# Performance work log

Hardware: AMD Instinct MI355X
Metric: run time of the kernel (lower is better)

The kernel has to match this reference:

```python
import jax, jax.numpy as jnp
import numpy as np

EPS = 0.2          # noise scale (init eps)
N_LAYERS = 3
LAYER_CL = 1
USER_NUM = 100000
ITEM_NUM = 50000
NNZ = 1200000
EMB = 64


def setup_inputs() -> dict:
    key = jax.random.key(0)
    k1, k2, k3, k4, k5, k6 = jax.random.split(key, 6)
    N = USER_NUM + ITEM_NUM
    user_emb = jax.random.normal(k1, (USER_NUM, EMB), dtype=jnp.float32)
    item_emb = jax.random.normal(k2, (ITEM_NUM, EMB), dtype=jnp.float32)
    adj_rows = jax.random.randint(k3, (NNZ,), 0, N, dtype=jnp.int32)
    adj_cols = jax.random.randint(k4, (NNZ,), 0, N, dtype=jnp.int32)
    adj_vals = jax.random.uniform(k5, (NNZ,), dtype=jnp.float32)
    noise = jax.random.uniform(k6, (N_LAYERS, N, EMB), dtype=jnp.float32)  # torch.rand_like per layer
    return {"user_emb": user_emb, "item_emb": item_emb, "adj_rows": adj_rows,
            "adj_cols": adj_cols, "adj_vals": adj_vals, "noise": noise}


def _l2_normalize(x):
    # F.normalize(x, dim=-1): x / max(||x||_2, 1e-12)
    n = jnp.sqrt(jnp.sum(x * x, axis=-1, keepdims=True))
    return x / jnp.maximum(n, 1e-12)


def reference(user_emb, item_emb, adj_rows, adj_cols, adj_vals, noise):
    N = user_emb.shape[0] + item_emb.shape[0]
    ego = jnp.concatenate([user_emb, item_emb], axis=0)  # [N, D]
    acc = jnp.zeros_like(ego)
    cl = ego
    for k in range(N_LAYERS):
        # SpMM: ego <- A @ ego (COO via gather + segment_sum)
        gathered = ego[adj_cols] * adj_vals[:, None]          # [nnz, D]
        ego = jax.ops.segment_sum(gathered, adj_rows, num_segments=N)
        # perturbed=True path: signed, l2-normalized uniform noise
        ego = ego + jnp.sign(ego) * _l2_normalize(noise[k]) * EPS
        acc = acc + ego
        if k == LAYER_CL - 1:
            cl = ego
    final = acc / N_LAYERS  # mean over layers (stack+mean fused)
    u = final[:user_emb.shape[0]]
    i = final[user_emb.shape[0]:]
    u_cl = cl[:user_emb.shape[0]]
    i_cl = cl[user_emb.shape[0]:]
    return (u, i, u_cl, i_cl)
```

## Files before the change

kernel.cpp:

```cpp
#include <hip/hip_runtime.h>

#define EPSV 0.2f
#define USER_NUM 100000
#define ITEM_NUM 50000
#define NTOT 150000
#define NNZ_CNT 1200000
#define EMB 64

#define RPB 128
#define NBUCK ((NTOT + RPB - 1) / RPB)
#define BLKA 128
#define SLICE_E (NNZ_CNT / BLKA)

typedef float v4f __attribute__((ext_vector_type(4)));
typedef int   v2i __attribute__((ext_vector_type(2)));


__global__ __launch_bounds__(256) void bucket_count_kernel(const int* __restrict__ rows,
                                                           int* __restrict__ bcount) {
    __shared__ int lh[NBUCK];
    const int t = threadIdx.x, blk = blockIdx.x;
    for (int b = t; b < NBUCK; b += 256) lh[b] = 0;
    __syncthreads();
    const int e0 = blk * SLICE_E;
    for (int e = e0 + t; e < e0 + SLICE_E; e += 256)
        atomicAdd(&lh[rows[e] >> 7], 1);
    __syncthreads();
    int* out = bcount + (size_t)blk * NBUCK;
    for (int b = t; b < NBUCK; b += 256) out[b] = lh[b];
}

__global__ __launch_bounds__(1024) void bucket_scan_kernel(int* __restrict__ bcount,
                                                           int* __restrict__ bucketStart) {
    __shared__ int tot[NBUCK];
    __shared__ int wsums[16];
    const int t = threadIdx.x;
    for (int b = t; b < NBUCK; b += 1024) {
        int run = 0;
        int* col = bcount + b;
        #pragma unroll 8
        for (int blk = 0; blk < BLKA; ++blk) {
            int v = col[(size_t)blk * NBUCK];
            col[(size_t)blk * NBUCK] = run;
            run += v;
        }
        tot[b] = run;
    }
    __syncthreads();
    int e0 = 2 * t, e1 = 2 * t + 1;
    int c0 = (e0 < NBUCK) ? tot[e0] : 0;
    int c1 = (e1 < NBUCK) ? tot[e1] : 0;
    int v = c0 + c1;
    int lane = t & 63, wid = t >> 6;
    int inc = v;
    #pragma unroll
    for (int off = 1; off < 64; off <<= 1) {
        int x = __shfl_up(inc, off, 64);
        if (lane >= off) inc += x;
    }
    if (lane == 63) wsums[wid] = inc;
    __syncthreads();
    if (t < 16) {
        int w = wsums[t];
        #pragma unroll
        for (int off = 1; off < 16; off <<= 1) {
            int x = __shfl_up(w, off, 64);
            if (t >= off) w += x;
        }
        wsums[t] = w;
    }
    __syncthreads();
    int waveoff = (wid > 0) ? wsums[wid - 1] : 0;
    int excl = waveoff + inc - v;
    if (e0 < NBUCK) bucketStart[e0] = excl;
    if (e1 < NBUCK) bucketStart[e1] = excl + c0;
    if (t == 0) bucketStart[NBUCK] = NNZ_CNT;
}

__global__ __launch_bounds__(256) void bucket_scatter_kernel(const int* __restrict__ rows,
                                                             const int* __restrict__ cols,
                                                             const float* __restrict__ vals,
                                                             const int* __restrict__ bcount,
                                                             const int* __restrict__ bucketStart,
                                                             int2* __restrict__ ebuf) {
    __shared__ int cur[NBUCK];
    const int t = threadIdx.x, blk = blockIdx.x;
    const int* mine = bcount + (size_t)blk * NBUCK;
    for (int b = t; b < NBUCK; b += 256) cur[b] = bucketStart[b] + mine[b];
    __syncthreads();
    const int e0 = blk * SLICE_E;
    for (int e = e0 + t; e < e0 + SLICE_E; e += 256) {
        int r = rows[e];
        int pos = atomicAdd(&cur[r >> 7], 1);
        ebuf[pos] = make_int2(cols[e] | ((r & 127) << 20), __float_as_int(vals[e]));
    }
}

__global__ __launch_bounds__(256) void bucket_csr_kernel(const int2* __restrict__ ebuf,
                                                         const int* __restrict__ bucketStart,
                                                         int2* __restrict__ rowrange,
                                                         int2* __restrict__ csr) {
    __shared__ int h[RPB];
    __shared__ int c[RPB];
    __shared__ int wst[4];
    const int t = threadIdx.x, b = blockIdx.x;
    const int base = bucketStart[b];
    const int n = bucketStart[b + 1] - base;
    if (t < RPB) h[t] = 0;
    __syncthreads();
    for (int i = t; i < n; i += 256)
        atomicAdd(&h[(ebuf[base + i].x >> 20) & 127], 1);
    __syncthreads();
    int lane = t & 63, wid = t >> 6;
    int v = (t < RPB) ? h[t] : 0;
    int inc = v;
    #pragma unroll
    for (int off = 1; off < 64; off <<= 1) {
        int x = __shfl_up(inc, off, 64);
        if (lane >= off) inc += x;
    }
    if (lane == 63) wst[wid] = inc;
    __syncthreads();
    int woff = (wid == 1) ? wst[0] : 0;
    int excl = woff + inc - v;
    if (t < RPB) {
        c[t] = excl;
        int r0 = b * RPB + t;
        if (r0 < NTOT) rowrange[r0] = make_int2(base + excl, base + excl + v);
    }
    __syncthreads();
    for (int i = t; i < n; i += 256) {
        int2 cc = ebuf[base + i];
        int lr = (cc.x >> 20) & 127;
        int pos = atomicAdd(&c[lr], 1);
        csr[base + pos] = make_int2(cc.x & 0xFFFFF, cc.y);
    }
}

template <bool CONCAT, bool FINAL_MODE>
__global__ void spmm_perturb_kernel(const float* __restrict__ src,
                                    const float* __restrict__ user_emb,
                                    const float* __restrict__ item_emb,
                                    const int2* __restrict__ rowrange,
                                    const int2* __restrict__ csr,
                                    const float* __restrict__ noise_k,
                                    const float* __restrict__ e1,
                                    const float* __restrict__ e2,
                                    float* __restrict__ out) {
    int wid = threadIdx.x >> 6;
    int lane = threadIdx.x & 63;
    int rsub = lane >> 4;
    int q = lane & 15;
    int row = blockIdx.x * 16 + wid * 4 + rsub;
    if (row >= NTOT) return;
    int2 rr = rowrange[row];
    int beg = rr.x, end = rr.y;
    size_t rowoff = (size_t)row * EMB;
    v4f nv = __builtin_nontemporal_load((const v4f*)(noise_k + rowoff) + q);
    v4f a1 = (v4f)(0.f);
    v4f a2 = (v4f)(0.f);
    if constexpr (FINAL_MODE) {
        a1 = __builtin_nontemporal_load((const v4f*)(e1 + rowoff) + q);
        a2 = ((const v4f*)(e2 + rowoff))[q];
    }
    v4f acc = (v4f)(0.f);
    for (int j = beg; j < end; j += 8) {
        int cb[8];
        float vb[8];
        #pragma unroll
        for (int u = 0; u < 8; ++u) {
            int jj = j + u;
            int idx = (jj < end) ? jj : (end - 1);
            v2i ee = __builtin_nontemporal_load((const v2i*)csr + idx);
            cb[u] = ee.x;
            vb[u] = (jj < end) ? __int_as_float(ee.y) : 0.f;
        }
        #pragma unroll
        for (int u = 0; u < 8; ++u) {
            int c = cb[u];
            const float* base;
            if (CONCAT)
                base = (c < USER_NUM) ? (user_emb + (size_t)c * EMB)
                                      : (item_emb + (size_t)(c - USER_NUM) * EMB);
            else
                base = src + (size_t)c * EMB;
            v4f x = ((const v4f*)base)[q];
            acc.x = fmaf(vb[u], x.x, acc.x);
            acc.y = fmaf(vb[u], x.y, acc.y);
            acc.z = fmaf(vb[u], x.z, acc.z);
            acc.w = fmaf(vb[u], x.w, acc.w);
        }
    }
    float s = nv.x * nv.x + nv.y * nv.y + nv.z * nv.z + nv.w * nv.w;
    #pragma unroll
    for (int off = 8; off > 0; off >>= 1) s += __shfl_xor(s, off, 64);
    float scale = EPSV / fmaxf(sqrtf(s), 1e-12f);
    auto pert = [&](float a, float n) {
        float sg = (a > 0.f) ? 1.f : ((a < 0.f) ? -1.f : 0.f);
        return fmaf(sg * scale, n, a);
    };
    v4f y;
    y.x = pert(acc.x, nv.x);
    y.y = pert(acc.y, nv.y);
    y.z = pert(acc.z, nv.z);
    y.w = pert(acc.w, nv.w);
    if constexpr (FINAL_MODE) {
        const float third = 1.f / 3.f;
        v4f f = (a1 + a2 + y) * third;
        __builtin_nontemporal_store(f, (v4f*)(out + rowoff) + q);
    } else {
        ((v4f*)(out + rowoff))[q] = y;
    }
}

extern "C" void kernel_launch(void* const* d_in, const int* in_sizes, int n_in,
                              void* d_out, int out_size, void* d_ws, size_t ws_size,
                              hipStream_t stream) {
    const float* user_emb = (const float*)d_in[0];
    const float* item_emb = (const float*)d_in[1];
    const int*   adj_rows = (const int*)d_in[2];
    const int*   adj_cols = (const int*)d_in[3];
    const float* adj_vals = (const float*)d_in[4];
    const float* noise    = (const float*)d_in[5];

    float* out_final = (float*)d_out;
    float* out_cl    = (float*)d_out + (size_t)NTOT * EMB;

    char* p = (char*)d_ws;
    float* wsA      = (float*)p;  p += (size_t)NTOT * EMB * sizeof(float);
    int2*  rowrange = (int2*)p;   p += (size_t)NTOT * sizeof(int2);
    int2*  csr      = (int2*)p;   p += (size_t)NNZ_CNT * sizeof(int2);

    char* q = (char*)wsA;
    int2* ebuf        = (int2*)q;  q += (size_t)NNZ_CNT * sizeof(int2);
    int*  bcount      = (int*)q;   q += (size_t)BLKA * NBUCK * sizeof(int);
    int*  bucketStart = (int*)q;   q += (size_t)(NBUCK + 1) * sizeof(int);

    bucket_count_kernel<<<BLKA, 256, 0, stream>>>(adj_rows, bcount);
    bucket_scan_kernel<<<1, 1024, 0, stream>>>(bcount, bucketStart);
    bucket_scatter_kernel<<<BLKA, 256, 0, stream>>>(adj_rows, adj_cols, adj_vals,
                                                    bcount, bucketStart, ebuf);
    bucket_csr_kernel<<<NBUCK, 256, 0, stream>>>(ebuf, bucketStart, rowrange, csr);

    const int spmm_blocks = (NTOT + 15) / 16;
    const size_t NE = (size_t)NTOT * EMB;

    spmm_perturb_kernel<true, false><<<spmm_blocks, 256, 0, stream>>>(
        nullptr, user_emb, item_emb, rowrange, csr, noise + 0 * NE,
        nullptr, nullptr, out_cl);
    spmm_perturb_kernel<false, false><<<spmm_blocks, 256, 0, stream>>>(
        out_cl, nullptr, nullptr, rowrange, csr, noise + 1 * NE,
        nullptr, nullptr, wsA);
    spmm_perturb_kernel<false, true><<<spmm_blocks, 256, 0, stream>>>(
        wsA, nullptr, nullptr, rowrange, csr, noise + 2 * NE,
        out_cl, wsA, out_final);
}
```

Before: 452.9 us.

## Fuse bucket scan into scatter and load CSR edges cooperatively via shuffles

Removes the single-block bucket_scan kernel. Each scatter block now redundantly computes the column prefix over all per-block bucket counts, plus a block-wide exclusive scan of the bucket totals, so the serial single-block launch disappears. The cost is that every block re-reads the whole count matrix from L2. In the SpMM kernels, each 16-lane row group now loads up to 16 edges cooperatively with one load per lane and broadcasts them with shuffles. This replaces the redundant per-lane 8-edge loads, but swaps a fixed unrolled loop for a runtime-bounded one, which may reduce how many gathers are in flight at once.

```diff
diff --git a/kernel.cpp b/kernel.cpp
--- a/kernel.cpp
+++ b/kernel.cpp
@@ -30,64 +30,67 @@
     for (int b = t; b < NBUCK; b += 256) out[b] = lh[b];
 }
 
-__global__ __launch_bounds__(1024) void bucket_scan_kernel(int* __restrict__ bcount,
-                                                           int* __restrict__ bucketStart) {
-    __shared__ int tot[NBUCK];
-    __shared__ int wsums[16];
-    const int t = threadIdx.x;
-    for (int b = t; b < NBUCK; b += 1024) {
-        int run = 0;
-        int* col = bcount + b;
-        #pragma unroll 8
-        for (int blk = 0; blk < BLKA; ++blk) {
-            int v = col[(size_t)blk * NBUCK];
-            col[(size_t)blk * NBUCK] = run;
-            run += v;
-        }
-        tot[b] = run;
-    }
-    __syncthreads();
-    int e0 = 2 * t, e1 = 2 * t + 1;
-    int c0 = (e0 < NBUCK) ? tot[e0] : 0;
-    int c1 = (e1 < NBUCK) ? tot[e1] : 0;
-    int v = c0 + c1;
-    int lane = t & 63, wid = t >> 6;
-    int inc = v;
-    #pragma unroll
-    for (int off = 1; off < 64; off <<= 1) {
-        int x = __shfl_up(inc, off, 64);
-        if (lane >= off) inc += x;
-    }
-    if (lane == 63) wsums[wid] = inc;
-    __syncthreads();
-    if (t < 16) {
-        int w = wsums[t];
-        #pragma unroll
-        for (int off = 1; off < 16; off <<= 1) {
-            int x = __shfl_up(w, off, 64);
-            if (t >= off) w += x;
-        }
-        wsums[t] = w;
-    }
-    __syncthreads();
-    int waveoff = (wid > 0) ? wsums[wid - 1] : 0;
-    int excl = waveoff + inc - v;
-    if (e0 < NBUCK) bucketStart[e0] = excl;
-    if (e1 < NBUCK) bucketStart[e1] = excl + c0;
-    if (t == 0) bucketStart[NBUCK] = NNZ_CNT;
-}
-
 __global__ __launch_bounds__(256) void bucket_scatter_kernel(const int* __restrict__ rows,
                                                              const int* __restrict__ cols,
                                                              const float* __restrict__ vals,
                                                              const int* __restrict__ bcount,
-                                                             const int* __restrict__ bucketStart,
+                                                             int* __restrict__ bucketStart,
                                                              int2* __restrict__ ebuf) {
     __shared__ int cur[NBUCK];
+    __shared__ int tot[NBUCK];
+    __shared__ int bst[NBUCK];
+    __shared__ int wsum[4];
+    __shared__ int wpre[4];
     const int t = threadIdx.x, blk = blockIdx.x;
-    const int* mine = bcount + (size_t)blk * NBUCK;
-    for (int b = t; b < NBUCK; b += 256) cur[b] = bucketStart[b] + mine[b];
-    __syncthreads();
+
+    for (int b = t; b < NBUCK; b += 256) {
+        int run = 0, pre = 0;
+        for (int blkp = 0; blkp < BLKA; ++blkp) {
+            if (blkp == blk) pre = run;
+            run += bcount[(size_t)blkp * NBUCK + b];
+        }
+        cur[b] = pre;
+        tot[b] = run;
+    }
+    __syncthreads();
+
+    int c0 = t * 5;
+    int lsum = 0;
+    #pragma unroll
+    for (int k = 0; k < 5; ++k) {
+        int b = c0 + k;
+        if (b < NBUCK) lsum += tot[b];
+    }
+    int lane = t & 63, wid = t >> 6;
+    int inc = lsum;
+    #pragma unroll
+    for (int off = 1; off < 64; off <<= 1) {
+        int x = __shfl_up(inc, off, 64);
+        if (lane >= off) inc += x;
+    }
+    if (lane == 63) wsum[wid] = inc;
+    __syncthreads();
+    if (t == 0) {
+        int run = 0;
+        #pragma unroll
+        for (int w = 0; w < 4; ++w) { wpre[w] = run; run += wsum[w]; }
+    }
+    __syncthreads();
+    int excl = wpre[wid] + inc - lsum;
+    #pragma unroll
+    for (int k = 0; k < 5; ++k) {
+        int b = c0 + k;
+        if (b < NBUCK) { bst[b] = excl; excl += tot[b]; }
+    }
+    __syncthreads();
+
+    for (int b = t; b < NBUCK; b += 256) cur[b] += bst[b];
+    if (blk == 0) {
+        for (int b = t; b < NBUCK; b += 256) bucketStart[b] = bst[b];
+        if (t == 0) bucketStart[NBUCK] = NNZ_CNT;
+    }
+    __syncthreads();
+
     const int e0 = blk * SLICE_E;
     for (int e = e0 + t; e < e0 + SLICE_E; e += 256) {
         int r = rows[e];
@@ -163,21 +166,16 @@
         a1 = __builtin_nontemporal_load((const v4f*)(e1 + rowoff) + q);
         a2 = ((const v4f*)(e2 + rowoff))[q];
     }
+    const int grp = rsub << 4;
     v4f acc = (v4f)(0.f);
-    for (int j = beg; j < end; j += 8) {
-        int cb[8];
-        float vb[8];
-        #pragma unroll
-        for (int u = 0; u < 8; ++u) {
-            int jj = j + u;
-            int idx = (jj < end) ? jj : (end - 1);
-            v2i ee = __builtin_nontemporal_load((const v2i*)csr + idx);
-            cb[u] = ee.x;
-            vb[u] = (jj < end) ? __int_as_float(ee.y) : 0.f;
-        }
-        #pragma unroll
-        for (int u = 0; u < 8; ++u) {
-            int c = cb[u];
+    for (int j = beg; j < end; j += 16) {
+        int jj = j + q;
+        v2i my = (v2i)(0);
+        if (jj < end) my = __builtin_nontemporal_load((const v2i*)csr + jj);
+        int nval = end - j; nval = (nval > 16) ? 16 : nval;
+        for (int u = 0; u < nval; ++u) {
+            int c = __shfl(my.x, grp + u, 64);
+            float vv = __int_as_float(__shfl(my.y, grp + u, 64));
             const float* base;
             if (CONCAT)
                 base = (c < USER_NUM) ? (user_emb + (size_t)c * EMB)
@@ -185,10 +183,10 @@
             else
                 base = src + (size_t)c * EMB;
             v4f x = ((const v4f*)base)[q];
-            acc.x = fmaf(vb[u], x.x, acc.x);
-            acc.y = fmaf(vb[u], x.y, acc.y);
-            acc.z = fmaf(vb[u], x.z, acc.z);
-            acc.w = fmaf(vb[u], x.w, acc.w);
+            acc.x = fmaf(vv, x.x, acc.x);
+            acc.y = fmaf(vv, x.y, acc.y);
+            acc.z = fmaf(vv, x.z, acc.z);
+            acc.w = fmaf(vv, x.w, acc.w);
         }
     }
     float s = nv.x * nv.x + nv.y * nv.y + nv.z * nv.z + nv.w * nv.w;
@@ -237,7 +235,6 @@
     int*  bucketStart = (int*)q;   q += (size_t)(NBUCK + 1) * sizeof(int);
 
     bucket_count_kernel<<<BLKA, 256, 0, stream>>>(adj_rows, bcount);
-    bucket_scan_kernel<<<1, 1024, 0, stream>>>(bcount, bucketStart);
     bucket_scatter_kernel<<<BLKA, 256, 0, stream>>>(adj_rows, adj_cols, adj_vals,
                                                     bcount, bucketStart, ebuf);
     bucket_csr_kernel<<<NBUCK, 256, 0, stream>>>(ebuf, bucketStart, rowrange, csr);
```

Result: no change. 454.7 us (+0.4%).
